# Kernel tuning notes

Measured on AMD Instinct MI355X. Metric: run time of the kernel, lower is better.

The kernel has to match this reference:

```python
import jax, jax.numpy as jnp
import numpy as np

HID = 64      # LSTM hidden size
UH_LEN = 15   # unit-hydrograph length (days)
N_INC = 4     # SAC-SMA sub-steps per day

# (name, lo, hi) -> sigmoid-scaled physical parameter ranges
PARAM_SPECS = [
    ("HAMON_COEF", 0.5, 2.0),
    ("SCF", 0.7, 1.4), ("PXTEMP", -2.0, 2.0), ("MFMAX", 0.5, 2.0), ("MFMIN", 0.05, 0.49),
    ("UADJ", 0.03, 0.19), ("MBASE", 0.0, 1.0), ("TIPM", 0.1, 1.0), ("PLWHC", 0.02, 0.3),
    ("NMF", 0.05, 0.5), ("DAYGM", 0.0, 0.3),
    ("UZTWM", 10.0, 300.0), ("UZFWM", 5.0, 150.0), ("LZTWM", 10.0, 500.0), ("LZFPM", 10.0, 1000.0),
    ("LZFSM", 5.0, 400.0), ("UZK", 0.1, 0.75), ("LZPK", 0.001, 0.05), ("LZSK", 0.01, 0.35),
    ("ZPERC", 5.0, 350.0), ("REXP", 1.0, 5.0), ("PFREE", 0.0, 0.8), ("PCTIM", 0.0, 0.1),
    ("ADIMP", 0.0, 0.4), ("RIVA", 0.0, 0.2), ("SIDE", 0.0, 0.5), ("RSERV", 0.0, 0.4),
    ("THETA_C", 0.0, 1.0), ("UH_N", 1.0, 6.0), ("UH_TAU", 0.5, 5.0),
]


def parameter_net(x_dyn, x_static, Wih, Whh, b_lstm, Ws, bs, Wout, bout):
    """gA: LSTM over dynamic inputs + static encoder -> per-unit physical params."""
    N = x_dyn.shape[0]
    h0 = jnp.zeros((N, HID), x_dyn.dtype)

    def step(carry, xt):
        h, c = carry
        z = xt @ Wih.T + h @ Whh.T + b_lstm
        i, f, g, o = jnp.split(z, 4, axis=-1)
        c = jax.nn.sigmoid(f) * c + jax.nn.sigmoid(i) * jnp.tanh(g)
        h = jax.nn.sigmoid(o) * jnp.tanh(c)
        return (h, c), None

    (h, _), _ = jax.lax.scan(step, (h0, h0), jnp.swapaxes(x_dyn, 0, 1))
    s = jnp.tanh(x_static @ Ws.T + bs)
    raw = jnp.concatenate([h, s], axis=-1) @ Wout.T + bout  # (N, n_params)
    g = jax.nn.sigmoid(raw)
    return {name: lo + g[:, k] * (hi - lo) for k, (name, lo, hi) in enumerate(PARAM_SPECS)}


def hamon_pet(tavg, doyf, lat_rad, coef):
    decl = 0.4093 * jnp.sin(2.0 * jnp.pi / 365.0 * doyf - 1.405)
    cosw = jnp.clip(-jnp.tan(lat_rad[:, None]) * jnp.tan(decl), -0.9999, 0.9999)
    daylen = jnp.arccos(cosw) * 24.0 / jnp.pi                   # hours
    esat = 0.6108 * jnp.exp(17.27 * tavg / (tavg + 237.3))      # kPa
    pet = coef[:, None] * 29.8 * daylen * esat / (tavg + 273.2)
    return jnp.maximum(pet, 0.0)


def run_snow17(prcp, tavg, doyf, elev_m, p):
    SCF, PXTEMP, MFMAX, MFMIN = p['SCF'], p['PXTEMP'], p['MFMAX'], p['MFMIN']
    UADJ, MBASE, TIPM, PLWHC = p['UADJ'], p['MBASE'], p['TIPM'], p['PLWHC']
    NMF, DAYGM = p['NMF'], p['DAYGM']
    pa_fac = jnp.exp(-elev_m / 8434.0)  # atmospheric pressure ratio with elevation

    def step(carry, inp):
        wi, wq, ati = carry
        pr, ta, dy = inp
        is_snow = ta <= PXTEMP
        ps = jnp.where(is_snow, pr * SCF, 0.0)
        prain = jnp.where(is_snow, 0.0, pr)
        wi = wi + ps
        mf = 0.5 * (MFMAX + MFMIN) + 0.5 * (MFMAX - MFMIN) * jnp.sin(2.0 * jnp.pi * dy / 366.0)
        ati = ati + TIPM * (jnp.minimum(ta, 0.0) - ati)
        mros = UADJ * pa_fac * jnp.maximum(ta, 0.0) * jnp.where((~is_snow) & (wi > 0.0), prain, 0.0) * 0.0125
        melt = jnp.clip(mf * jnp.maximum(ta - MBASE, 0.0) + mros - NMF * jnp.maximum(-ati, 0.0), 0.0, wi)
        wi = wi - melt
        gm = jnp.minimum(DAYGM, wi)
        wi = wi - gm
        rain_on_pack = jnp.where(wi > 0.0, prain, 0.0)
        rain_free = prain - rain_on_pack
        wq = wq + melt + rain_on_pack
        out = jnp.maximum(wq - PLWHC * wi, 0.0)
        wq = wq - out
        return (wi, wq, ati), out + gm + rain_free

    z = jnp.zeros_like(p['SCF'])
    _, eff = jax.lax.scan(step, (z, z, z), (prcp.T, tavg.T, doyf.T))
    return eff.T  # (N, T)


def run_sacsma(pav, ep, p, n_inc):
    UZTWM, UZFWM, LZTWM = p['UZTWM'], p['UZFWM'], p['LZTWM']
    LZFPM, LZFSM, UZK = p['LZFPM'], p['LZFSM'], p['UZK']
    LZPK, LZSK, ZPERC, REXP = p['LZPK'], p['LZSK'], p['ZPERC'], p['REXP']
    PFREE, PCTIM, ADIMP, SIDE = p['PFREE'], p['PCTIM'], p['ADIMP'], p['SIDE']
    dt = 1.0 / n_inc
    percm = LZFPM * LZPK + LZFSM * LZSK
    lz_max = LZTWM + LZFPM + LZFSM

    def step(carry, inp):
        uztwc, uzfwc, lztwc, lzfpc, lzfsc, adimc = carry
        pr, e = inp
        # evapotranspiration
        e1 = jnp.minimum(e * uztwc / UZTWM, uztwc); uztwc = uztwc - e1
        red = e - e1
        e2 = jnp.minimum(red, uzfwc); uzfwc = uzfwc - e2; red = red - e2
        e3 = jnp.minimum(red * lztwc / (UZTWM + LZTWM), lztwc); lztwc = lztwc - e3
        # impervious + additional impervious area
        roimp = pr * PCTIM
        padimp = pr * ADIMP
        adimc = adimc + padimp
        adsur = padimp * jnp.clip(adimc / (UZTWM + LZTWM), 0.0, 1.0) ** 2
        adimc = jnp.minimum(adimc - adsur, UZTWM + LZTWM)
        surf = roimp + adsur
        base = jnp.zeros_like(pr)
        pinc = pr * (1.0 - PCTIM - ADIMP) * dt
        for _ in range(n_inc):  # unrolled sub-steps (n_inc is small, static)
            bfp = lzfpc * LZPK * dt; bfs = lzfsc * LZSK * dt
            lzfpc = lzfpc - bfp; lzfsc = lzfsc - bfs
            base = base + (bfp + bfs) / (1.0 + SIDE)
            qif = uzfwc * UZK * dt; uzfwc = uzfwc - qif; surf = surf + qif
            lz_def = (LZTWM - lztwc) + (LZFPM - lzfpc) + (LZFSM - lzfsc)
            defr = jnp.clip(lz_def / lz_max, 1e-6, 1.0)
            perc = percm * (1.0 + ZPERC * defr ** REXP) * dt * uzfwc / UZFWM
            perc = jnp.minimum(jnp.minimum(perc, uzfwc), jnp.maximum(lz_def, 0.0))
            uzfwc = uzfwc - perc
            pfree = perc * PFREE
            lztwc = lztwc + perc - pfree
            ex = jnp.maximum(lztwc - LZTWM, 0.0); lztwc = lztwc - ex; pfree = pfree + ex
            dp = jnp.maximum(LZFPM - lzfpc, 0.0); ds = jnp.maximum(LZFSM - lzfsc, 0.0)
            fr = dp / jnp.maximum(dp + ds, 1e-6)
            lzfpc = lzfpc + pfree * fr; lzfsc = lzfsc + pfree * (1.0 - fr)
            exp_ = jnp.maximum(lzfpc - LZFPM, 0.0); lzfpc = lzfpc - exp_; lzfsc = lzfsc + exp_
            exs = jnp.maximum(lzfsc - LZFSM, 0.0); lzfsc = lzfsc - exs; surf = surf + exs
            uztwc = uztwc + pinc
            exu = jnp.maximum(uztwc - UZTWM, 0.0); uztwc = uztwc - exu
            uzfwc = uzfwc + exu
            exf = jnp.maximum(uzfwc - UZFWM, 0.0); uzfwc = uzfwc - exf
            surf = surf + exf
        return (uztwc, uzfwc, lztwc, lzfpc, lzfsc, adimc), (surf, base)

    init = (0.5 * UZTWM, 0.5 * UZFWM, 0.5 * LZTWM, 0.5 * LZFPM, 0.5 * LZFSM, 0.5 * (UZTWM + LZTWM))
    _, (surf, base) = jax.lax.scan(step, init, (pav.T, ep.T))
    return surf.T, base.T  # (N, T)


def route_lohmann(surf, base, uh_n, uh_tau):
    """Gamma-shaped unit hydrograph per unit; causal convolution over time."""
    t = jnp.arange(1.0, UH_LEN + 1.0)  # (L,)
    w = t[None, :] ** (uh_n[:, None] - 1.0) * jnp.exp(-t[None, :] / uh_tau[:, None])
    uh = w / jnp.sum(w, axis=1, keepdims=True)  # (N, L)
    T = surf.shape[1]
    pad = jnp.pad(surf, ((0, 0), (UH_LEN - 1, 0)))
    q = sum(uh[:, l:l + 1] * pad[:, UH_LEN - 1 - l: UH_LEN - 1 - l + T] for l in range(UH_LEN))
    return q + base


def setup_inputs() -> dict:
    key = jax.random.key(0)
    ks = jax.random.split(key, 13)
    N, T, D_DYN, D_STAT, B = 4000, 730, 8, 16, 200
    NP = len(PARAM_SPECS)
    return {
        'x_dyn': jax.random.normal(ks[0], (N, T, D_DYN), jnp.float32),
        'x_static': jax.random.normal(ks[1], (N, D_STAT), jnp.float32),
        'prcp': 10.0 * jax.random.uniform(ks[2], (N, T), jnp.float32),
        'tavg': 5.0 + 8.0 * jax.random.normal(ks[3], (N, T), jnp.float32),
        'doy': jax.random.randint(ks[4], (N, T), 1, 367, jnp.int32),
        'elev_m': 2500.0 * jax.random.uniform(ks[5], (N,), jnp.float32),
        'lat_rad': 0.2 + 0.6 * jax.random.uniform(ks[6], (N,), jnp.float32),
        'area_weight': jax.random.uniform(ks[7], (N,), jnp.float32),
        'basin_index': jax.random.randint(ks[8], (N,), 0, B, jnp.int32),
        'n_basins': B,
        'Wih': 0.1 * jax.random.normal(ks[9], (4 * HID, D_DYN), jnp.float32),
        'Whh': 0.1 * jax.random.normal(ks[10], (4 * HID, HID), jnp.float32),
        'b_lstm': jnp.zeros((4 * HID,), jnp.float32),
        'Ws': 0.1 * jax.random.normal(ks[11], (HID, D_STAT), jnp.float32),
        'bs': jnp.zeros((HID,), jnp.float32),
        'Wout': 0.1 * jax.random.normal(ks[12], (NP, 2 * HID), jnp.float32),
        'bout': jnp.zeros((NP,), jnp.float32),
    }


def reference(x_dyn, x_static, prcp, tavg, doy, elev_m, lat_rad, area_weight,
              basin_index, n_basins, Wih, Whh, b_lstm, Ws, bs, Wout, bout):
    params = parameter_net(x_dyn, x_static, Wih, Whh, b_lstm, Ws, bs, Wout, bout)
    doyf = doy.astype(jnp.float32)
    pet = hamon_pet(tavg, doyf, lat_rad, params['HAMON_COEF'])
    effective_p = run_snow17(prcp, tavg, doyf, elev_m, params)
    surf, base = run_sacsma(effective_p, pet, params, N_INC)
    q_unit = route_lohmann(surf, base, params['UH_N'], params['UH_TAU'])
    w = area_weight[:, None]
    B = int(n_basins)
    q_gauge = jax.ops.segment_sum(q_unit * w, basin_index, num_segments=B)
    q_base_gauge = jax.ops.segment_sum(base * w, basin_index, num_segments=B)
    return q_gauge, q_base_gauge, q_unit
```

## Files before the change

### kernel.cpp

```cpp
#include <hip/hip_runtime.h>
#include <math.h>

#define HID 64
#define UH_LEN 15
#define N_INC 4

#define TWO_PI_365 0.0172142063f
#define TWO_PI_366 0.0171671554f
#define H24_PI     7.63943727f

typedef short short8 __attribute__((ext_vector_type(8)));
typedef float f32x4  __attribute__((ext_vector_type(4)));

__device__ __forceinline__ float frcp(float x){ return __builtin_amdgcn_rcpf(x); }
__device__ __forceinline__ float sigf(float x){ return frcp(1.0f + __expf(-x)); }
__device__ __forceinline__ float tanhfast(float x){ return 1.0f - 2.0f*frcp(__expf(2.0f*x)+1.0f); }

__device__ __forceinline__ unsigned short f2bf(float f){
    unsigned int u = __float_as_uint(f);
    u += 0x7FFF + ((u >> 16) & 1);
    return (unsigned short)(u >> 16);
}
__device__ __forceinline__ float bf2f(unsigned short h){
    return __uint_as_float(((unsigned int)h) << 16);
}

__device__ const float PLO[30] = {0.5f,0.7f,-2.0f,0.5f,0.05f,0.03f,0.0f,0.1f,0.02f,0.05f,0.0f,
                                  10.0f,5.0f,10.0f,10.0f,5.0f,0.1f,0.001f,0.01f,5.0f,1.0f,0.0f,
                                  0.0f,0.0f,0.0f,0.0f,0.0f,0.0f,1.0f,0.5f};
__device__ const float PHI[30] = {2.0f,1.4f,2.0f,2.0f,0.49f,0.19f,1.0f,1.0f,0.3f,0.5f,0.3f,
                                  300.0f,150.0f,500.0f,1000.0f,400.0f,0.75f,0.05f,0.35f,350.0f,5.0f,0.8f,
                                  0.1f,0.4f,0.2f,0.5f,0.4f,1.0f,6.0f,5.0f};
__device__ const float LOGT[15] = {0.0f,0.69314718f,1.09861229f,1.38629436f,1.60943791f,
                                   1.79175947f,1.94591015f,2.07944154f,2.19722458f,2.30258509f,
                                   2.39789527f,2.48490665f,2.56494936f,2.63905733f,2.70805020f};

__global__ void zero_kernel(float* __restrict__ p, int cnt){
    int i = blockIdx.x*256 + threadIdx.x;
    if (i < cnt) p[i] = 0.0f;
}

__global__ __launch_bounds__(256) void xpack_kernel(
    const float* __restrict__ x_dyn, unsigned short* __restrict__ xb, size_t NT)
{
    size_t i = (size_t)blockIdx.x*256 + threadIdx.x;
    if (i >= NT) return;
    const float4 a = ((const float4*)x_dyn)[2*i];
    const float4 b = ((const float4*)x_dyn)[2*i + 1];
    short8 o;
    o[0]=(short)f2bf(a.x); o[1]=(short)f2bf(a.y); o[2]=(short)f2bf(a.z); o[3]=(short)f2bf(a.w);
    o[4]=(short)f2bf(b.x); o[5]=(short)f2bf(b.y); o[6]=(short)f2bf(b.z); o[7]=(short)f2bf(b.w);
    ((short8*)xb)[i] = o;
}

template<bool XB>
__global__ __launch_bounds__(256, 1) void lstm_kernel(
    const float* __restrict__ x_dyn, const unsigned short* __restrict__ xb,
    const float* __restrict__ x_static,
    const float* __restrict__ Wih, const float* __restrict__ Whh,
    const float* __restrict__ b_lstm, const float* __restrict__ Ws,
    const float* __restrict__ bs, const float* __restrict__ Wout,
    const float* __restrict__ bout, float* __restrict__ params,
    int N, int T, int DSTAT)
{
    __shared__ unsigned short h_lds[2][16*64];
    __shared__ float s_sh[16*64];

    const int tid = threadIdx.x;
    const int wv  = tid >> 6;
    const int ln  = tid & 63;
    const int q   = ln >> 4;
    const int r16 = ln & 15;
    const int u0  = blockIdx.x * 16;

    short8 wf[4][3];
    float  bias[4];
    #pragma unroll
    for (int g = 0; g < 4; ++g) {
        const int n = 64*g + 16*wv + r16;
        bias[g] = b_lstm[n];
        #pragma unroll
        for (int kb = 0; kb < 3; ++kb) {
            short8 w;
            #pragma unroll
            for (int e = 0; e < 8; ++e) {
                int k = 32*kb + 8*q + e;
                float v = 0.0f;
                if (k < 64)      v = Whh[n*64 + k];
                else if (k < 72) v = Wih[n*8 + (k - 64)];
                w[e] = (short)f2bf(v);
            }
            wf[g][kb] = w;
        }
    }

    for (int i = tid; i < 2*16*64; i += 256) ((unsigned short*)h_lds)[i] = 0;
    __syncthreads();

    float c[4] = {0.f, 0.f, 0.f, 0.f};

    const int ux = min(u0 + r16, N-1);
    const int jj   = 16*wv + r16;
    const int swz0 = (q       ^ (r16 & 7)) << 3;
    const int swz1 = ((q + 4) ^ (r16 & 7)) << 3;

#define LSTM_STEP(T_CUR, RB, XREG)                                              \
    {                                                                           \
        short8 a0 = *(const short8*)&h_lds[RB][r16*64 + swz0];                  \
        short8 a1 = *(const short8*)&h_lds[RB][r16*64 + swz1];                  \
        short8 a2 = XREG;                                                       \
        if (q == 0)                                                             \
            XREG = *(const short8*)(xb + ((size_t)ux*T + min((T_CUR)+2, T-1))*8);\
        f32x4 acc[4];                                                           \
        _Pragma("unroll")                                                       \
        for (int gg = 0; gg < 4; ++gg) {                                        \
            f32x4 a; a[0]=bias[gg]; a[1]=bias[gg]; a[2]=bias[gg]; a[3]=bias[gg];\
            a = __builtin_amdgcn_mfma_f32_16x16x32_bf16(a2, wf[gg][2], a,0,0,0);\
            a = __builtin_amdgcn_mfma_f32_16x16x32_bf16(a0, wf[gg][0], a,0,0,0);\
            a = __builtin_amdgcn_mfma_f32_16x16x32_bf16(a1, wf[gg][1], a,0,0,0);\
            acc[gg] = a;                                                        \
        }                                                                       \
        _Pragma("unroll")                                                       \
        for (int r = 0; r < 4; ++r) {                                           \
            float iv = sigf(acc[0][r]);                                         \
            float fv = sigf(acc[1][r]);                                         \
            float gv = tanhfast(acc[2][r]);                                     \
            float ov = sigf(acc[3][r]);                                         \
            c[r] = fv*c[r] + iv*gv;                                             \
            float hv = ov*tanhfast(c[r]);                                       \
            int u = 4*q + r;                                                    \
            h_lds[(RB)^1][u*64 + (((jj>>3) ^ (u&7))<<3) + (jj&7)] = f2bf(hv);   \
        }                                                                       \
        asm volatile("s_waitcnt lgkmcnt(0)" ::: "memory");                      \
        __builtin_amdgcn_s_barrier();                                           \
    }

    if constexpr (XB) {
        short8 x0, x1;
        #pragma unroll
        for (int e = 0; e < 8; ++e) { x0[e] = 0; x1[e] = 0; }
        if (q == 0) {
            x0 = *(const short8*)(xb + ((size_t)ux*T)*8);
            x1 = *(const short8*)(xb + ((size_t)ux*T + min(1, T-1))*8);
        }
        int t = 0;
        for (; t + 1 < T; t += 2) {
            LSTM_STEP(t,   0, x0);
            LSTM_STEP(t+1, 1, x1);
        }
        if (t < T) LSTM_STEP(t, 0, x0);
    } else {
        float xf[8];
        if (q == 0) {
            const float* p = x_dyn + ((size_t)ux * T) * 8;
            #pragma unroll
            for (int e = 0; e < 8; ++e) xf[e] = p[e];
        }
        for (int t = 0; t < T; ++t) {
            short8 a2;
            #pragma unroll
            for (int e = 0; e < 8; ++e) a2[e] = (q == 0) ? (short)f2bf(xf[e]) : (short)0;
            const int rb = t & 1;
            short8 a0 = *(const short8*)&h_lds[rb][r16*64 + swz0];
            short8 a1 = *(const short8*)&h_lds[rb][r16*64 + swz1];
            if (q == 0 && t + 1 < T) {
                const float* p = x_dyn + ((size_t)ux * T + (t+1)) * 8;
                #pragma unroll
                for (int e = 0; e < 8; ++e) xf[e] = p[e];
            }
            f32x4 acc[4];
            #pragma unroll
            for (int g = 0; g < 4; ++g) {
                f32x4 a; a[0]=bias[g]; a[1]=bias[g]; a[2]=bias[g]; a[3]=bias[g];
                a = __builtin_amdgcn_mfma_f32_16x16x32_bf16(a2, wf[g][2], a, 0, 0, 0);
                a = __builtin_amdgcn_mfma_f32_16x16x32_bf16(a0, wf[g][0], a, 0, 0, 0);
                a = __builtin_amdgcn_mfma_f32_16x16x32_bf16(a1, wf[g][1], a, 0, 0, 0);
                acc[g] = a;
            }
            const int wb = rb ^ 1;
            #pragma unroll
            for (int r = 0; r < 4; ++r) {
                float iv = sigf(acc[0][r]);
                float fv = sigf(acc[1][r]);
                float gv = tanhfast(acc[2][r]);
                float ov = sigf(acc[3][r]);
                c[r] = fv*c[r] + iv*gv;
                float hv = ov*tanhfast(c[r]);
                int u = 4*q + r;
                h_lds[wb][u*64 + (((jj>>3) ^ (u&7))<<3) + (jj&7)] = f2bf(hv);
            }
            __syncthreads();
        }
    }
#undef LSTM_STEP

    const int fb = T & 1;
    for (int uu = 0; uu < 4; ++uu) {
        int ul = wv*4 + uu;
        int u  = min(u0 + ul, N-1);
        float a = bs[ln];
        for (int k = 0; k < DSTAT; ++k)
            a = fmaf(x_static[(size_t)u*DSTAT + k], Ws[ln*DSTAT + k], a);
        s_sh[ul*64 + ln] = tanhfast(a);
    }
    if (ln < 30) {
        for (int uu = 0; uu < 4; ++uu) {
            int ul = wv*4 + uu;
            int unit = u0 + ul;
            if (unit < N) {
                float raw = bout[ln];
                #pragma unroll 8
                for (int m = 0; m < 64; ++m) {
                    float hm = bf2f(h_lds[fb][ul*64 + (((m>>3) ^ (ul&7))<<3) + (m&7)]);
                    float sm = s_sh[ul*64 + m];
                    raw = fmaf(hm, Wout[ln*128 + m],      raw);
                    raw = fmaf(sm, Wout[ln*128 + 64 + m], raw);
                }
                float g = sigf(raw);
                params[ln*N + unit] = PLO[ln] + g*(PHI[ln] - PLO[ln]);
            }
        }
    }
}

__global__ __launch_bounds__(256) void pack_kernel(
    const float* __restrict__ prcp, const float* __restrict__ tavg,
    const int* __restrict__ doy, const float* __restrict__ lat_rad,
    const float* __restrict__ P,
    float4* __restrict__ pack, int N, int T)
{
    const int n = blockIdx.y;
    const int t = blockIdx.x*256 + threadIdx.x;
    if (t >= T) return;
    const float pr = prcp[(size_t)n*T + t];
    const float ta = tavg[(size_t)n*T + t];
    const float dy = (float)doy[(size_t)n*T + t];
    const float tanlat = __tanf(lat_rad[n]);
    const float HAMON  = P[n];
    const float MFMAX  = P[3*N + n], MFMIN = P[4*N + n];
    float decl  = 0.4093f*__sinf(TWO_PI_365*dy - 1.405f);
    float cosw  = fminf(fmaxf(-tanlat*__tanf(decl), -0.9999f), 0.9999f);
    float daylen= acosf(cosw)*H24_PI;
    float esat  = 0.6108f*__expf(17.27f*ta*frcp(ta + 237.3f));
    float pet   = fmaxf(HAMON*29.8f*daylen*esat*frcp(ta + 273.2f), 0.0f);
    float mf    = 0.5f*(MFMAX + MFMIN) + 0.5f*(MFMAX - MFMIN)*__sinf(TWO_PI_366*dy);
    pack[(size_t)n*T + t] = make_float4(pr, ta, pet, mf);
}

__global__ __launch_bounds__(64, 1) void physics_fast_kernel(
    const float* __restrict__ elev_m, const float* __restrict__ P,
    const float4* __restrict__ pack, float2* __restrict__ sbA, int N, int T)
{
    int n = blockIdx.x*64 + threadIdx.x;
    if (n >= N) return;

    const float SCF   = P[ 1*N+n], PXTEMP= P[ 2*N+n];
    const float MBASE = P[ 6*N+n], TIPM  = P[ 7*N+n], PLWHC = P[ 8*N+n];
    const float NMF   = P[ 9*N+n], DAYGM = P[10*N+n];
    const float UZTWM = P[11*N+n], UZFWM = P[12*N+n], LZTWM = P[13*N+n];
    const float LZFPM = P[14*N+n], LZFSM = P[15*N+n];
    const float UZK   = P[16*N+n], LZPK  = P[17*N+n], LZSK  = P[18*N+n];
    const float ZPERC = P[19*N+n], REXP  = P[20*N+n], PFREE = P[21*N+n];
    const float PCTIM = P[22*N+n], ADIMP = P[23*N+n], SIDE  = P[25*N+n];

    const float mrosk = P[5*N+n]*__expf(-elev_m[n]*(1.0f/8434.0f))*0.0125f;
    const float dtq   = 1.0f/(float)N_INC;
    const float kp = LZPK*dtq, ks = LZSK*dtq, ku = UZK*dtq;
    const float c1p = 1.f-kp, c1s = 1.f-ks, c1u = 1.f-ku, c1t = 1.f-TIPM;
    const float twm = UZTWM + LZTWM;
    const float iUZTWM = frcp(UZTWM), itwm = frcp(twm);
    const float lzmax  = LZTWM + LZFPM + LZFSM;
    const float ilzmax = frcp(lzmax);
    const float iside  = frcp(1.f + SIDE);
    const float pfac   = (1.f - PCTIM - ADIMP)*dtq;
    const float pm     = (LZFPM*LZPK + LZFSM*LZSK)*dtq*frcp(UZFWM);

    float wi = 0.f, wq = 0.f, ati = 0.f;
    float uztwc = .5f*UZTWM, uzfwc = .5f*UZFWM, lztwc = .5f*LZTWM;
    float lzfpc = .5f*LZFPM, lzfsc = .5f*LZFSM, adimc = .5f*twm;

    const float4* pk = pack + (size_t)n*T;
    float2*       sb = sbA  + (size_t)n*T;
    float4 cur = pk[0];
    float4 nx1 = pk[T > 1 ? 1 : 0];

    for (int t = 0; t < T; ++t) {
        float4 nx2 = pk[min(t + 2, T - 1)];
        const float pr = cur.x, ta = cur.y, pet = cur.z, mf = cur.w;

        const bool  is_snow = (ta <= PXTEMP);
        const float ps    = is_snow ? pr*SCF : 0.f;
        const float prain = is_snow ? 0.f : pr;
        const float tmros = mrosk*fmaxf(ta, 0.f)*prain;
        const float m0    = mf*fmaxf(ta - MBASE, 0.f);
        const float atia  = TIPM*fminf(ta, 0.f);
        const float me1   = fminf(pet*iUZTWM, 1.f);
        const float e1fac = 1.f - me1;

        ati = c1t*ati + atia;
        float wi1  = wi + ps;
        float mros = (!is_snow && wi1 > 0.f) ? tmros : 0.f;
        float melt = fminf(fmaxf(m0 + mros - NMF*fmaxf(-ati, 0.f), 0.f), wi1);
        float wi2  = wi1 - melt;
        float gm   = fminf(DAYGM, wi2);
        float wi3  = fmaxf(wi2 - DAYGM, 0.f);
        wi = wi3;
        float rop   = (wi3 > 0.f) ? prain : 0.f;
        float rfree = prain - rop;
        float wq1 = wq + melt + rop;
        float cap = PLWHC*wi3;
        float outq = fmaxf(wq1 - cap, 0.f);
        wq = fminf(wq1, cap);
        float eff = outq + gm + rfree;

        float red  = pet - uztwc*me1;
        uztwc = uztwc*e1fac;
        float red2 = fmaxf(red - uzfwc, 0.f);
        uzfwc = fmaxf(uzfwc - red, 0.f);
        lztwc = lztwc*(1.f - fminf(red2*itwm, 1.f));

        float roimp  = eff*PCTIM;
        float padimp = eff*ADIMP;
        float adimc1 = adimc + padimp;
        float ratio  = fminf(fmaxf(adimc1*itwm, 0.f), 1.f);
        float adsur  = padimp*ratio*ratio;
        adimc = fminf(adimc1 - adsur, twm);
        float surf = roimp + adsur;
        float base = 0.f;
        float pinc = eff*pfac;

        #pragma unroll
        for (int inc = 0; inc < N_INC; ++inc) {
            float bfp = lzfpc*kp, bfs = lzfsc*ks;
            lzfpc *= c1p; lzfsc *= c1s;
            base += (bfp + bfs)*iside;
            float qif = uzfwc*ku;
            uzfwc *= c1u;
            surf += qif;
            float lz_def = lzmax - (lztwc + (lzfpc + lzfsc));
            float defr = fminf(fmaxf(lz_def*ilzmax, 1e-6f), 1.f);
            float perc = pm*fmaf(ZPERC, __expf(REXP*__logf(defr)), 1.f)*uzfwc;
            perc = fminf(fminf(perc, uzfwc), fmaxf(lz_def, 0.f));
            uzfwc -= perc;
            float pfree0 = perc*PFREE;
            float lztwc1 = lztwc + perc - pfree0;
            float ex = fmaxf(lztwc1 - LZTWM, 0.f);
            lztwc = fminf(lztwc1, LZTWM);
            float pfree = pfree0 + ex;
            float dp  = fmaxf(LZFPM - lzfpc, 0.f);
            float dsx = fmaxf(LZFSM - lzfsc, 0.f);
            float fr  = dp*frcp(fmaxf(dp + dsx, 1e-6f));
            float lzfpc1 = lzfpc + pfree*fr;
            float lzfsc1 = lzfsc + pfree*(1.f - fr);
            float exq = fmaxf(lzfpc1 - LZFPM, 0.f);
            lzfpc = fminf(lzfpc1, LZFPM);
            float lzfsc2 = lzfsc1 + exq;
            float exs = fmaxf(lzfsc2 - LZFSM, 0.f);
            lzfsc = fminf(lzfsc2, LZFSM);
            surf += exs;
            float uztwc1 = uztwc + pinc;
            float exu = fmaxf(uztwc1 - UZTWM, 0.f);
            uztwc = fminf(uztwc1, UZTWM);
            float uzfwc1 = uzfwc + exu;
            float exf = fmaxf(uzfwc1 - UZFWM, 0.f);
            uzfwc = fminf(uzfwc1, UZFWM);
            surf += exf;
        }

        sb[t] = make_float2(surf, base);
        cur = nx1; nx1 = nx2;
    }
}

template<bool SPLIT>
__global__ __launch_bounds__(64, 1) void physics_kernel(
    const float* __restrict__ prcp, const float* __restrict__ tavg,
    const int*   __restrict__ doy,  const float* __restrict__ elev_m,
    const float* __restrict__ lat_rad, const float* __restrict__ area_w,
    const int*   __restrict__ basin_idx, const float* __restrict__ P,
    float* __restrict__ surfA, float* __restrict__ baseA,
    float* __restrict__ out, int N, int T, int B)
{
    int n = blockIdx.x*64 + threadIdx.x;
    if (n >= N) return;

    const float HAMON = P[ 0*N+n], SCF   = P[ 1*N+n], PXTEMP= P[ 2*N+n];
    const float MFMAX = P[ 3*N+n], MFMIN = P[ 4*N+n];
    const float MBASE = P[ 6*N+n], TIPM  = P[ 7*N+n], PLWHC = P[ 8*N+n];
    const float NMF   = P[ 9*N+n], DAYGM = P[10*N+n];
    const float UZTWM = P[11*N+n], UZFWM = P[12*N+n], LZTWM = P[13*N+n];
    const float LZFPM = P[14*N+n], LZFSM = P[15*N+n], UZK   = P[16*N+n];
    const float LZPK  = P[17*N+n], LZSK  = P[18*N+n], ZPERC = P[19*N+n];
    const float REXP  = P[20*N+n], PFREE = P[21*N+n], PCTIM = P[22*N+n];
    const float ADIMP = P[23*N+n], SIDE  = P[25*N+n];
    const float UH_N  = P[28*N+n], UH_TAU= P[29*N+n];

    const float mrosk  = P[5*N+n]*__expf(-elev_m[n]*(1.0f/8434.0f))*0.0125f;
    const float tanlat = __tanf(lat_rad[n]);
    const float wA     = area_w[n];
    const int   bi     = basin_idx[n];
    const float mfa = 0.5f*(MFMAX + MFMIN), mfb = 0.5f*(MFMAX - MFMIN);

    float uh[UH_LEN];
    float hist[UH_LEN-1];
    if (!SPLIT) {
        float uhs = 0.0f;
        const float inv_tau = frcp(UH_TAU);
        #pragma unroll
        for (int l = 0; l < UH_LEN; ++l) {
            uh[l] = __expf((UH_N - 1.0f)*LOGT[l] - (float)(l+1)*inv_tau);
            uhs += uh[l];
        }
        float inv_uhs = frcp(uhs);
        #pragma unroll
        for (int l = 0; l < UH_LEN; ++l) uh[l] *= inv_uhs;
        #pragma unroll
        for (int l = 0; l < UH_LEN-1; ++l) hist[l] = 0.0f;
    }

    const float dtq       = 1.0f / (float)N_INC;
    const float kp        = LZPK*dtq, ks = LZSK*dtq, ku = UZK*dtq;
    const float twm_sum   = UZTWM + LZTWM;
    const float inv_uztwm = frcp(UZTWM);
    const float inv_twm   = frcp(twm_sum);
    const float inv_lzmax = frcp(LZTWM + LZFPM + LZFSM);
    const float inv_side  = frcp(1.0f + SIDE);
    const float pinc_fac  = (1.0f - PCTIM - ADIMP)*dtq;
    const float pm        = (LZFPM*LZPK + LZFSM*LZSK)*dtq*frcp(UZFWM);

    float wi = 0.0f, wq = 0.0f, ati = 0.0f;
    float uztwc = 0.5f*UZTWM, uzfwc = 0.5f*UZFWM, lztwc = 0.5f*LZTWM;
    float lzfpc = 0.5f*LZFPM, lzfsc = 0.5f*LZFSM, adimc = 0.5f*twm_sum;

    float* q_gauge = out;
    float* q_base  = out + (size_t)B*T;
    float* q_unit  = out + (size_t)2*B*T;

    float pr_c = prcp[(size_t)n*T];
    float ta_c = tavg[(size_t)n*T];
    float dy0 = (float)doy[(size_t)n*T];
    float decl0 = 0.4093f*__sinf(TWO_PI_365*dy0 - 1.405f);
    float cosw0 = fminf(fmaxf(-tanlat*__tanf(decl0), -0.9999f), 0.9999f);
    float pet_c = fmaxf(HAMON*29.8f*(acosf(cosw0)*H24_PI)
                        *0.6108f*__expf(17.27f*ta_c*frcp(ta_c + 237.3f))
                        *frcp(ta_c + 273.2f), 0.0f);
    float mf_c  = mfa + mfb*__sinf(TWO_PI_366*dy0);

    for (int t = 0; t < T; ++t) {
        const int tn = min(t + 1, T - 1);
        float pr_n = prcp[(size_t)n*T + tn];
        float ta_n = tavg[(size_t)n*T + tn];
        float dy_n = (float)doy[(size_t)n*T + tn];
        const float pr = pr_c, ta = ta_c, pet = pet_c, mf = mf_c;

        bool is_snow = (ta <= PXTEMP);
        float ps    = is_snow ? pr*SCF : 0.0f;
        float prain = is_snow ? 0.0f   : pr;
        wi += ps;
        ati += TIPM*(fminf(ta, 0.0f) - ati);
        float mros = mrosk*fmaxf(ta, 0.0f)*((!is_snow && wi > 0.0f) ? prain : 0.0f);
        float melt = fminf(fmaxf(mf*fmaxf(ta - MBASE, 0.0f) + mros - NMF*fmaxf(-ati, 0.0f), 0.0f), wi);
        wi -= melt;
        float gm = fminf(DAYGM, wi);
        wi -= gm;
        float rop   = (wi > 0.0f) ? prain : 0.0f;
        float rfree = prain - rop;
        wq += melt + rop;
        float outq = fmaxf(wq - PLWHC*wi, 0.0f);
        wq -= outq;
        float eff = outq + gm + rfree;

        float e1 = fminf(pet*uztwc*inv_uztwm, uztwc);
        uztwc -= e1;
        float red = pet - e1;
        float e2 = fminf(red, uzfwc);
        uzfwc -= e2; red -= e2;
        float e3 = fminf(red*lztwc*inv_twm, lztwc);
        lztwc -= e3;
        float roimp  = eff*PCTIM;
        float padimp = eff*ADIMP;
        adimc += padimp;
        float ratio = fminf(fmaxf(adimc*inv_twm, 0.0f), 1.0f);
        float adsur = padimp*ratio*ratio;
        adimc = fminf(adimc - adsur, twm_sum);
        float surf = roimp + adsur;
        float base = 0.0f;
        float pinc = eff*pinc_fac;
        #pragma unroll
        for (int inc = 0; inc < N_INC; ++inc) {
            float bfp = lzfpc*kp;
            float bfs = lzfsc*ks;
            lzfpc -= bfp; lzfsc -= bfs;
            base += (bfp + bfs)*inv_side;
            float qif = uzfwc*ku;
            uzfwc -= qif; surf += qif;
            float lz_def = (LZTWM - lztwc) + (LZFPM - lzfpc) + (LZFSM - lzfsc);
            float defr = fminf(fmaxf(lz_def*inv_lzmax, 1e-6f), 1.0f);
            float perc = pm*fmaf(ZPERC, __expf(REXP*__logf(defr)), 1.0f)*uzfwc;
            perc = fminf(fminf(perc, uzfwc), fmaxf(lz_def, 0.0f));
            uzfwc -= perc;
            float pfree = perc*PFREE;
            lztwc += perc - pfree;
            float ex = fmaxf(lztwc - LZTWM, 0.0f);
            lztwc -= ex; pfree += ex;
            float dp  = fmaxf(LZFPM - lzfpc, 0.0f);
            float dsx = fmaxf(LZFSM - lzfsc, 0.0f);
            float fr  = dp*frcp(fmaxf(dp + dsx, 1e-6f));
            lzfpc += pfree*fr;
            lzfsc += pfree*(1.0f - fr);
            float exq = fmaxf(lzfpc - LZFPM, 0.0f);
            lzfpc -= exq; lzfsc += exq;
            float exs = fmaxf(lzfsc - LZFSM, 0.0f);
            lzfsc -= exs; surf += exs;
            uztwc += pinc;
            float exu = fmaxf(uztwc - UZTWM, 0.0f);
            uztwc -= exu; uzfwc += exu;
            float exf = fmaxf(uzfwc - UZFWM, 0.0f);
            uzfwc -= exf; surf += exf;
        }

        if (SPLIT) {
            surfA[(size_t)n*T + t] = surf;
            baseA[(size_t)n*T + t] = base;
        } else {
            float qv = uh[0]*surf;
            #pragma unroll
            for (int l = 1; l < UH_LEN; ++l) qv = fmaf(uh[l], hist[l-1], qv);
            #pragma unroll
            for (int l = UH_LEN-2; l >= 1; --l) hist[l] = hist[l-1];
            hist[0] = surf;
            qv += base;
            q_unit[(size_t)n*T + t] = qv;
            atomicAdd(&q_gauge[(size_t)bi*T + t], qv*wA);
            atomicAdd(&q_base [(size_t)bi*T + t], base*wA);
        }

        float decl = 0.4093f*__sinf(TWO_PI_365*dy_n - 1.405f);
        float cosw = fminf(fmaxf(-tanlat*__tanf(decl), -0.9999f), 0.9999f);
        pet_c = fmaxf(HAMON*29.8f*(acosf(cosw)*H24_PI)
                      *0.6108f*__expf(17.27f*ta_n*frcp(ta_n + 237.3f))
                      *frcp(ta_n + 273.2f), 0.0f);
        mf_c = mfa + mfb*__sinf(TWO_PI_366*dy_n);
        pr_c = pr_n; ta_c = ta_n;
    }
}

template<bool PACKED>
__global__ __launch_bounds__(256) void route_kernel(
    const float2* __restrict__ sbA,
    const float* __restrict__ surfA, const float* __restrict__ baseA,
    const float* __restrict__ P, const float* __restrict__ area_w,
    const int* __restrict__ basin_idx,
    float* __restrict__ out, int N, int T, int B)
{
    __shared__ float uh_sh[UH_LEN];
    __shared__ float wA_sh;
    __shared__ int   bi_sh;

    const int n = blockIdx.y;
    const int t = blockIdx.x*256 + threadIdx.x;

    if (threadIdx.x == 0) {
        float UH_N = P[28*N + n], UH_TAU = P[29*N + n];
        float inv_tau = frcp(UH_TAU);
        float tmp[UH_LEN], s = 0.f;
        #pragma unroll
        for (int l = 0; l < UH_LEN; ++l) {
            tmp[l] = __expf((UH_N - 1.0f)*LOGT[l] - (float)(l+1)*inv_tau);
            s += tmp[l];
        }
        float is = frcp(s);
        #pragma unroll
        for (int l = 0; l < UH_LEN; ++l) uh_sh[l] = tmp[l]*is;
        wA_sh = area_w[n];
        bi_sh = basin_idx[n];
    }
    __syncthreads();
    if (t >= T) return;

    float base, acc = 0.f;
    if (PACKED) {
        const float2* sb = sbA + (size_t)n*T;
        base = sb[t].y;
        #pragma unroll
        for (int l = 0; l < UH_LEN; ++l) {
            int tt = t - l;
            if (tt >= 0) acc = fmaf(uh_sh[l], sb[tt].x, acc);
        }
    } else {
        base = baseA[(size_t)n*T + t];
        #pragma unroll
        for (int l = 0; l < UH_LEN; ++l) {
            int tt = t - l;
            if (tt >= 0) acc = fmaf(uh_sh[l], surfA[(size_t)n*T + tt], acc);
        }
    }
    const float qv = acc + base;

    float* q_gauge = out;
    float* q_base  = out + (size_t)B*T;
    float* q_unit  = out + (size_t)2*B*T;

    q_unit[(size_t)n*T + t] = qv;
    atomicAdd(&q_gauge[(size_t)bi_sh*T + t], qv*wA_sh);
    atomicAdd(&q_base [(size_t)bi_sh*T + t], base*wA_sh);
}

static inline size_t align256(size_t x){ return (x + 255) & ~(size_t)255; }

extern "C" void kernel_launch(void* const* d_in, const int* in_sizes, int n_in,
                              void* d_out, int out_size, void* d_ws, size_t ws_size,
                              hipStream_t stream) {
    const float* x_dyn    = (const float*)d_in[0];
    const float* x_static = (const float*)d_in[1];
    const float* prcp     = (const float*)d_in[2];
    const float* tavg     = (const float*)d_in[3];
    const int*   doy      = (const int*)  d_in[4];
    const float* elev_m   = (const float*)d_in[5];
    const float* lat_rad  = (const float*)d_in[6];
    const float* area_w   = (const float*)d_in[7];
    const int*   basin_ix = (const int*)  d_in[8];
    const float* Wih      = (const float*)d_in[10];
    const float* Whh      = (const float*)d_in[11];
    const float* b_lstm   = (const float*)d_in[12];
    const float* Ws       = (const float*)d_in[13];
    const float* bs       = (const float*)d_in[14];
    const float* Wout     = (const float*)d_in[15];
    const float* bout     = (const float*)d_in[16];

    const int N = in_sizes[7];
    const int T = in_sizes[2] / N;
    const int DSTAT = in_sizes[1] / N;
    const size_t NT = (size_t)N * T;
    const int B = (out_size - (int)NT) / (2 * T);

    char* wsb = (char*)d_ws;
    float* params = (float*)wsb;
    const size_t off_prm = align256(30*(size_t)N*sizeof(float));

    const size_t off_xb0   = off_prm;
    const size_t off_pack0 = align256(off_xb0 + NT*16);
    const size_t off_sb0   = align256(off_pack0 + NT*16);
    const size_t need0     = off_sb0 + NT*8;
    const size_t off_pack1 = off_prm;
    const size_t off_sb1   = align256(off_pack1 + NT*16);
    const size_t need1     = off_sb1 + NT*8;
    const size_t off_surf2 = off_prm;
    const size_t off_base2 = off_surf2 + NT*4;
    const size_t need2     = off_base2 + NT*4;

    const int tier = (ws_size >= need0) ? 0 : (ws_size >= need1) ? 1 :
                     (ws_size >= need2) ? 2 : 3;

    float* out = (float*)d_out;
    const int zc = 2 * B * T;
    zero_kernel<<<(zc + 255)/256, 256, 0, stream>>>(out, zc);

    const int blocks_lstm = (N + 15) / 16;
    const int pblocks = (N + 63) / 64;
    dim3 rg((T + 255)/256, N);

    if (tier == 0) {
        unsigned short* xbp = (unsigned short*)(wsb + off_xb0);
        float4* pack = (float4*)(wsb + off_pack0);
        float2* sbA  = (float2*)(wsb + off_sb0);
        xpack_kernel<<<(int)((NT + 255)/256), 256, 0, stream>>>(x_dyn, xbp, NT);
        lstm_kernel<true><<<blocks_lstm, 256, 0, stream>>>(
            x_dyn, xbp, x_static, Wih, Whh, b_lstm, Ws, bs, Wout, bout,
            params, N, T, DSTAT);
        pack_kernel<<<rg, 256, 0, stream>>>(prcp, tavg, doy, lat_rad, params, pack, N, T);
        physics_fast_kernel<<<pblocks, 64, 0, stream>>>(elev_m, params, pack, sbA, N, T);
        route_kernel<true><<<rg, 256, 0, stream>>>(sbA, nullptr, nullptr, params, area_w,
                                                   basin_ix, out, N, T, B);
    } else if (tier == 1) {
        float4* pack = (float4*)(wsb + off_pack1);
        float2* sbA  = (float2*)(wsb + off_sb1);
        lstm_kernel<false><<<blocks_lstm, 256, 0, stream>>>(
            x_dyn, nullptr, x_static, Wih, Whh, b_lstm, Ws, bs, Wout, bout,
            params, N, T, DSTAT);
        pack_kernel<<<rg, 256, 0, stream>>>(prcp, tavg, doy, lat_rad, params, pack, N, T);
        physics_fast_kernel<<<pblocks, 64, 0, stream>>>(elev_m, params, pack, sbA, N, T);
        route_kernel<true><<<rg, 256, 0, stream>>>(sbA, nullptr, nullptr, params, area_w,
                                                   basin_ix, out, N, T, B);
    } else if (tier == 2) {
        float* surfA = (float*)(wsb + off_surf2);
        float* baseA = (float*)(wsb + off_base2);
        lstm_kernel<false><<<blocks_lstm, 256, 0, stream>>>(
            x_dyn, nullptr, x_static, Wih, Whh, b_lstm, Ws, bs, Wout, bout,
            params, N, T, DSTAT);
        physics_kernel<true><<<pblocks, 64, 0, stream>>>(
            prcp, tavg, doy, elev_m, lat_rad, area_w, basin_ix, params,
            surfA, baseA, out, N, T, B);
        route_kernel<false><<<rg, 256, 0, stream>>>(nullptr, surfA, baseA, params, area_w,
                                                    basin_ix, out, N, T, B);
    } else {
        lstm_kernel<false><<<blocks_lstm, 256, 0, stream>>>(
            x_dyn, nullptr, x_static, Wih, Whh, b_lstm, Ws, bs, Wout, bout,
            params, N, T, DSTAT);
        physics_kernel<false><<<pblocks, 64, 0, stream>>>(
            prcp, tavg, doy, elev_m, lat_rad, area_w, basin_ix, params,
            nullptr, nullptr, out, N, T, B);
    }
}
```

Before: 1.043 ms.

## Fuse zeroing, forcing pack and bf16 packing into one pre-LSTM kernel

Merges the output zeroing, the x_dyn bf16 packing and the forcing pack into a single prep kernel that runs before the LSTM. To make that possible, the per-unit parameters (HAMON coefficient and melt-factor range) are taken out of the pack and applied inside the physics kernel. The aim is to cut launch count and to remove the pack kernel that sat between the LSTM and the physics kernels. It also reorganises the LSTM gate math to share reciprocals, and replaces exp/log with __powf in the percolation step. The risks are a larger combined grid and small numerical differences from the rearranged activations.

```diff
diff --git a/kernel.cpp b/kernel.cpp
--- a/kernel.cpp
+++ b/kernel.cpp
@@ -40,17 +40,42 @@
     if (i < cnt) p[i] = 0.0f;
 }
 
-__global__ __launch_bounds__(256) void xpack_kernel(
-    const float* __restrict__ x_dyn, unsigned short* __restrict__ xb, size_t NT)
+__global__ __launch_bounds__(256) void prep_kernel(
+    const float* __restrict__ x_dyn,
+    const float* __restrict__ prcp, const float* __restrict__ tavg,
+    const int* __restrict__ doy, const float* __restrict__ lat_rad,
+    float* __restrict__ outz, unsigned short* __restrict__ xb,
+    float4* __restrict__ pack, int zc, size_t NT, int T)
 {
-    size_t i = (size_t)blockIdx.x*256 + threadIdx.x;
-    if (i >= NT) return;
-    const float4 a = ((const float4*)x_dyn)[2*i];
-    const float4 b = ((const float4*)x_dyn)[2*i + 1];
-    short8 o;
-    o[0]=(short)f2bf(a.x); o[1]=(short)f2bf(a.y); o[2]=(short)f2bf(a.z); o[3]=(short)f2bf(a.w);
-    o[4]=(short)f2bf(b.x); o[5]=(short)f2bf(b.y); o[6]=(short)f2bf(b.z); o[7]=(short)f2bf(b.w);
-    ((short8*)xb)[i] = o;
+    size_t idx = (size_t)blockIdx.x*256 + threadIdx.x;
+    if (idx < (size_t)zc) { outz[idx] = 0.0f; return; }
+    idx -= zc;
+    if (idx < NT) {
+        const size_t i = idx;
+        const int n = (int)(i / (size_t)T);
+        const float pr = prcp[i];
+        const float ta = tavg[i];
+        const float dy = (float)doy[i];
+        const float tanlat = __tanf(lat_rad[n]);
+        float decl  = 0.4093f*__sinf(TWO_PI_365*dy - 1.405f);
+        float cosw  = fminf(fmaxf(-tanlat*__tanf(decl), -0.9999f), 0.9999f);
+        float daylen= acosf(cosw)*H24_PI;
+        float esat  = 0.6108f*__expf(17.27f*ta*frcp(ta + 237.3f));
+        float pet0  = 29.8f*daylen*esat*frcp(ta + 273.2f);
+        float s366  = __sinf(TWO_PI_366*dy);
+        pack[i] = make_float4(pr, ta, pet0, s366);
+        return;
+    }
+    idx -= NT;
+    if (xb && idx < NT) {
+        const size_t i = idx;
+        const float4 a = ((const float4*)x_dyn)[2*i];
+        const float4 b = ((const float4*)x_dyn)[2*i + 1];
+        short8 o;
+        o[0]=(short)f2bf(a.x); o[1]=(short)f2bf(a.y); o[2]=(short)f2bf(a.z); o[3]=(short)f2bf(a.w);
+        o[4]=(short)f2bf(b.x); o[5]=(short)f2bf(b.y); o[6]=(short)f2bf(b.z); o[7]=(short)f2bf(b.w);
+        ((short8*)xb)[i] = o;
+    }
 }
 
 template<bool XB>
@@ -122,12 +147,15 @@
         }                                                                       \
         _Pragma("unroll")                                                       \
         for (int r = 0; r < 4; ++r) {                                           \
-            float iv = sigf(acc[0][r]);                                         \
-            float fv = sigf(acc[1][r]);                                         \
-            float gv = tanhfast(acc[2][r]);                                     \
-            float ov = sigf(acc[3][r]);                                         \
-            c[r] = fv*c[r] + iv*gv;                                             \
-            float hv = ov*tanhfast(c[r]);                                       \
+            float e_i = __expf(-acc[0][r]);                                     \
+            float e_f = __expf(-acc[1][r]);                                     \
+            float e_g = __expf(2.f*acc[2][r]);                                  \
+            float e_o = __expf(-acc[3][r]);                                     \
+            float fv  = frcp(1.f + e_f);                                        \
+            float ig  = (e_g - 1.f)*frcp((e_g + 1.f)*(1.f + e_i));              \
+            c[r] = fv*c[r] + ig;                                                \
+            float e_c = __expf(2.f*c[r]);                                       \
+            float hv  = (e_c - 1.f)*frcp((e_c + 1.f)*(1.f + e_o));              \
             int u = 4*q + r;                                                    \
             h_lds[(RB)^1][u*64 + (((jj>>3) ^ (u&7))<<3) + (jj&7)] = f2bf(hv);   \
         }                                                                       \
@@ -223,30 +251,6 @@
     }
 }
 
-__global__ __launch_bounds__(256) void pack_kernel(
-    const float* __restrict__ prcp, const float* __restrict__ tavg,
-    const int* __restrict__ doy, const float* __restrict__ lat_rad,
-    const float* __restrict__ P,
-    float4* __restrict__ pack, int N, int T)
-{
-    const int n = blockIdx.y;
-    const int t = blockIdx.x*256 + threadIdx.x;
-    if (t >= T) return;
-    const float pr = prcp[(size_t)n*T + t];
-    const float ta = tavg[(size_t)n*T + t];
-    const float dy = (float)doy[(size_t)n*T + t];
-    const float tanlat = __tanf(lat_rad[n]);
-    const float HAMON  = P[n];
-    const float MFMAX  = P[3*N + n], MFMIN = P[4*N + n];
-    float decl  = 0.4093f*__sinf(TWO_PI_365*dy - 1.405f);
-    float cosw  = fminf(fmaxf(-tanlat*__tanf(decl), -0.9999f), 0.9999f);
-    float daylen= acosf(cosw)*H24_PI;
-    float esat  = 0.6108f*__expf(17.27f*ta*frcp(ta + 237.3f));
-    float pet   = fmaxf(HAMON*29.8f*daylen*esat*frcp(ta + 273.2f), 0.0f);
-    float mf    = 0.5f*(MFMAX + MFMIN) + 0.5f*(MFMAX - MFMIN)*__sinf(TWO_PI_366*dy);
-    pack[(size_t)n*T + t] = make_float4(pr, ta, pet, mf);
-}
-
 __global__ __launch_bounds__(64, 1) void physics_fast_kernel(
     const float* __restrict__ elev_m, const float* __restrict__ P,
     const float4* __restrict__ pack, float2* __restrict__ sbA, int N, int T)
@@ -254,7 +258,9 @@
     int n = blockIdx.x*64 + threadIdx.x;
     if (n >= N) return;
 
+    const float HAMON = P[ 0*N+n];
     const float SCF   = P[ 1*N+n], PXTEMP= P[ 2*N+n];
+    const float MFMAX = P[ 3*N+n], MFMIN = P[ 4*N+n];
     const float MBASE = P[ 6*N+n], TIPM  = P[ 7*N+n], PLWHC = P[ 8*N+n];
     const float NMF   = P[ 9*N+n], DAYGM = P[10*N+n];
     const float UZTWM = P[11*N+n], UZFWM = P[12*N+n], LZTWM = P[13*N+n];
@@ -264,6 +270,7 @@
     const float PCTIM = P[22*N+n], ADIMP = P[23*N+n], SIDE  = P[25*N+n];
 
     const float mrosk = P[5*N+n]*__expf(-elev_m[n]*(1.0f/8434.0f))*0.0125f;
+    const float mfa = 0.5f*(MFMAX + MFMIN), mfb = 0.5f*(MFMAX - MFMIN);
     const float dtq   = 1.0f/(float)N_INC;
     const float kp = LZPK*dtq, ks = LZSK*dtq, ku = UZK*dtq;
     const float c1p = 1.f-kp, c1s = 1.f-ks, c1u = 1.f-ku, c1t = 1.f-TIPM;
@@ -286,7 +293,9 @@
 
     for (int t = 0; t < T; ++t) {
         float4 nx2 = pk[min(t + 2, T - 1)];
-        const float pr = cur.x, ta = cur.y, pet = cur.z, mf = cur.w;
+        const float pr = cur.x, ta = cur.y;
+        const float pet = HAMON*fmaxf(cur.z, 0.f);
+        const float mf  = fmaf(mfb, cur.w, mfa);
 
         const bool  is_snow = (ta <= PXTEMP);
         const float ps    = is_snow ? pr*SCF : 0.f;
@@ -339,7 +348,7 @@
             surf += qif;
             float lz_def = lzmax - (lztwc + (lzfpc + lzfsc));
             float defr = fminf(fmaxf(lz_def*ilzmax, 1e-6f), 1.f);
-            float perc = pm*fmaf(ZPERC, __expf(REXP*__logf(defr)), 1.f)*uzfwc;
+            float perc = pm*fmaf(ZPERC, __powf(defr, REXP), 1.f)*uzfwc;
             perc = fminf(fminf(perc, uzfwc), fmaxf(lz_def, 0.f));
             uzfwc -= perc;
             float pfree0 = perc*PFREE;
@@ -654,35 +663,34 @@
 
     float* out = (float*)d_out;
     const int zc = 2 * B * T;
-    zero_kernel<<<(zc + 255)/256, 256, 0, stream>>>(out, zc);
 
     const int blocks_lstm = (N + 15) / 16;
     const int pblocks = (N + 63) / 64;
     dim3 rg((T + 255)/256, N);
 
-    if (tier == 0) {
-        unsigned short* xbp = (unsigned short*)(wsb + off_xb0);
-        float4* pack = (float4*)(wsb + off_pack0);
-        float2* sbA  = (float2*)(wsb + off_sb0);
-        xpack_kernel<<<(int)((NT + 255)/256), 256, 0, stream>>>(x_dyn, xbp, NT);
-        lstm_kernel<true><<<blocks_lstm, 256, 0, stream>>>(
-            x_dyn, xbp, x_static, Wih, Whh, b_lstm, Ws, bs, Wout, bout,
-            params, N, T, DSTAT);
-        pack_kernel<<<rg, 256, 0, stream>>>(prcp, tavg, doy, lat_rad, params, pack, N, T);
-        physics_fast_kernel<<<pblocks, 64, 0, stream>>>(elev_m, params, pack, sbA, N, T);
-        route_kernel<true><<<rg, 256, 0, stream>>>(sbA, nullptr, nullptr, params, area_w,
-                                                   basin_ix, out, N, T, B);
-    } else if (tier == 1) {
-        float4* pack = (float4*)(wsb + off_pack1);
-        float2* sbA  = (float2*)(wsb + off_sb1);
-        lstm_kernel<false><<<blocks_lstm, 256, 0, stream>>>(
-            x_dyn, nullptr, x_static, Wih, Whh, b_lstm, Ws, bs, Wout, bout,
-            params, N, T, DSTAT);
-        pack_kernel<<<rg, 256, 0, stream>>>(prcp, tavg, doy, lat_rad, params, pack, N, T);
+    if (tier == 0 || tier == 1) {
+        unsigned short* xbp = (tier == 0) ? (unsigned short*)(wsb + off_xb0) : nullptr;
+        float4* pack = (float4*)(wsb + (tier == 0 ? off_pack0 : off_pack1));
+        float2* sbA  = (float2*)(wsb + (tier == 0 ? off_sb0   : off_sb1));
+
+        const size_t total = (size_t)zc + NT + (xbp ? NT : 0);
+        prep_kernel<<<(int)((total + 255)/256), 256, 0, stream>>>(
+            x_dyn, prcp, tavg, doy, lat_rad, out, xbp, pack, zc, NT, T);
+
+        if (tier == 0)
+            lstm_kernel<true><<<blocks_lstm, 256, 0, stream>>>(
+                x_dyn, xbp, x_static, Wih, Whh, b_lstm, Ws, bs, Wout, bout,
+                params, N, T, DSTAT);
+        else
+            lstm_kernel<false><<<blocks_lstm, 256, 0, stream>>>(
+                x_dyn, nullptr, x_static, Wih, Whh, b_lstm, Ws, bs, Wout, bout,
+                params, N, T, DSTAT);
+
         physics_fast_kernel<<<pblocks, 64, 0, stream>>>(elev_m, params, pack, sbA, N, T);
         route_kernel<true><<<rg, 256, 0, stream>>>(sbA, nullptr, nullptr, params, area_w,
                                                    basin_ix, out, N, T, B);
     } else if (tier == 2) {
+        zero_kernel<<<(zc + 255)/256, 256, 0, stream>>>(out, zc);
         float* surfA = (float*)(wsb + off_surf2);
         float* baseA = (float*)(wsb + off_base2);
         lstm_kernel<false><<<blocks_lstm, 256, 0, stream>>>(
@@ -694,6 +702,7 @@
         route_kernel<false><<<rg, 256, 0, stream>>>(nullptr, surfA, baseA, params, area_w,
                                                     basin_ix, out, N, T, B);
     } else {
+        zero_kernel<<<(zc + 255)/256, 256, 0, stream>>>(out, zc);
         lstm_kernel<false><<<blocks_lstm, 256, 0, stream>>>(
             x_dyn, nullptr, x_static, Wih, Whh, b_lstm, Ws, bs, Wout, bout,
             params, N, T, DSTAT);
```

Measured after the change: 1.819 ms. +74.4%, slower.
